# Performance work log

Measured on AMD Instinct MI355X. Metric: run time of the kernel, lower is better.

The kernel has to match this reference:

```python
import jax, jax.numpy as jnp
import numpy as np

S = 8192        # seq_length
H2 = 1024       # 2 * lstm_hidden_size
A = 2048        # attention_hidden_size
E = 768         # embedding_dim == pos_embedding_dim


def _bahdanau_weights(sentence, length, ctx, W_s, b_s, W_c, b_c, v, b_v):
    # sentence: [1, S, H2], ctx: [1, E_ctx]
    u = jnp.einsum('bsh,ha->bsa', sentence, W_s) + b_s \
        + (ctx @ W_c + b_c)[:, None, :]                    # [1, S, A]
    e = jnp.einsum('bsa,a->bs', jnp.tanh(u), v) + b_v       # [1, S]
    mask = jnp.arange(S)[None, :] >= length[:, None]        # [1, S] key mask
    e = jnp.where(mask, -jnp.inf, e)
    all_inf = jnp.all(mask, axis=1)                         # [1]
    # guard fully-masked rows so softmax stays finite, then zero them (matches torch)
    e_safe = jnp.where(all_inf[:, None], jnp.zeros_like(e), e)
    w = jax.nn.softmax(e_safe, axis=1)
    return jnp.where(all_inf[:, None], 0.0, w)              # [1, S]


def setup_inputs() -> dict:
    key = jax.random.key(0)
    ks = jax.random.split(key, 24)
    f = jax.random.normal
    sc_s = 1.0 / np.sqrt(H2)
    sc_c = 1.0 / np.sqrt(E)
    sc_v = 1.0 / np.sqrt(A)
    inp = {
        'sentence': f(ks[0], (1, S, H2), jnp.float32),
        'length': jax.random.randint(ks[1], (1,), 0, S),
        'pos_embedding': f(ks[2], (1, E), jnp.float32),
        'cardinal_phrase_embedding': f(ks[3], (1, E), jnp.float32),
        'headline_embedding': f(ks[4], (1, E), jnp.float32),
    }
    i = 5
    for tag in ('p', 'c', 'h'):
        inp[f'W_sent_{tag}'] = f(ks[i], (H2, A), jnp.float32) * sc_s; i += 1
        inp[f'b_sent_{tag}'] = f(ks[i], (A,), jnp.float32) * sc_s; i += 1
        inp[f'W_ctx_{tag}'] = f(ks[i], (E, A), jnp.float32) * sc_c; i += 1
        inp[f'b_ctx_{tag}'] = f(ks[i], (A,), jnp.float32) * sc_c; i += 1
        inp[f'v_{tag}'] = f(ks[i], (A,), jnp.float32) * sc_v; i += 1
        inp[f'bv_{tag}'] = f(ks[i], (), jnp.float32) * sc_v; i += 1
    return inp


def reference(sentence, length, pos_embedding, cardinal_phrase_embedding,
              headline_embedding,
              W_sent_p, b_sent_p, W_ctx_p, b_ctx_p, v_p, bv_p,
              W_sent_c, b_sent_c, W_ctx_c, b_ctx_c, v_c, bv_c,
              W_sent_h, b_sent_h, W_ctx_h, b_ctx_h, v_h, bv_h):
    w_pos = _bahdanau_weights(sentence, length, pos_embedding,
                              W_sent_p, b_sent_p, W_ctx_p, b_ctx_p, v_p, bv_p)
    w_card = _bahdanau_weights(sentence, length, cardinal_phrase_embedding,
                               W_sent_c, b_sent_c, W_ctx_c, b_ctx_c, v_c, bv_c)
    w_head = _bahdanau_weights(sentence, length, headline_embedding,
                               W_sent_h, b_sent_h, W_ctx_h, b_ctx_h, v_h, bv_h)
    fused = (w_pos + w_card + w_head) / 3.0                 # [1, S]
    return jnp.einsum('bs,bsh->bh', fused, sentence)        # [1, H2]
```

## Files before the change

kernel.cpp:

```cpp
#include <hip/hip_runtime.h>
#include <hip/hip_bf16.h>
#include <stdint.h>


namespace {

constexpr int S = 8192;
constexpr int H = 1024;
constexpr int A = 2048;
constexpr int E = 768;

typedef __bf16 bf16x8 __attribute__((ext_vector_type(8)));
typedef float f32x4 __attribute__((ext_vector_type(4)));

__device__ __forceinline__ void gl_lds16(const void* g, void* l) {
  __builtin_amdgcn_global_load_lds(
      (const __attribute__((address_space(1))) void*)g,
      (__attribute__((address_space(3))) void*)l, 16, 0, 0);
}

__global__ __launch_bounds__(256)
void k_prep(const float* __restrict__ sentence, __bf16* __restrict__ sentB,
            const float* __restrict__ Wp, const float* __restrict__ Wc_s,
            const float* __restrict__ Wh, __bf16* __restrict__ WtB,
            const float* __restrict__ ctx_p, const float* __restrict__ ctx_c,
            const float* __restrict__ ctx_h,
            const float* __restrict__ Wcx_p, const float* __restrict__ Wcx_c,
            const float* __restrict__ Wcx_h,
            const float* __restrict__ bs_p, const float* __restrict__ bs_c,
            const float* __restrict__ bs_h,
            const float* __restrict__ bc_p, const float* __restrict__ bc_c,
            const float* __restrict__ bc_h,
            float* __restrict__ ctxb) {
  __shared__ float tile[64][65];
  int b = blockIdx.x;
  int t = threadIdx.x;

  if (b < 4096) {
    int g = b * 256 + t;
    const float4* s4 = (const float4*)sentence + (size_t)g * 2;
    float4 a = s4[0], c = s4[1];
    bf16x8 o;
    o[0] = (__bf16)a.x; o[1] = (__bf16)a.y; o[2] = (__bf16)a.z; o[3] = (__bf16)a.w;
    o[4] = (__bf16)c.x; o[5] = (__bf16)c.y; o[6] = (__bf16)c.z; o[7] = (__bf16)c.w;
    *((bf16x8*)sentB + g) = o;
  } else if (b < 5632) {
    int r = b - 4096;
    int head = r >> 9; r &= 511;
    const float* W = head == 0 ? Wp : (head == 1 ? Wc_s : Wh);
    __bf16* dst = WtB + (size_t)head * A * H;
    int a0 = (r & 31) * 64;
    int k0 = (r >> 5) * 64;
#pragma unroll
    for (int i = 0; i < 16; ++i) {
      int idx = t + i * 256;
      int rr = idx >> 6, cc = idx & 63;
      tile[cc][rr] = W[(size_t)(k0 + rr) * A + a0 + cc];
    }
    __syncthreads();
#pragma unroll
    for (int i = 0; i < 16; ++i) {
      int idx = t + i * 256;
      int al = idx >> 6, kl = idx & 63;
      dst[(size_t)(a0 + al) * H + k0 + kl] = (__bf16)tile[al][kl];
    }
  } else {
    int r = b - 5632;
    int head = r / 192; r %= 192;
    int ablk = r & 7;
    int echk = r >> 3;
    const float* ctx = head == 0 ? ctx_p : (head == 1 ? ctx_c : ctx_h);
    const float* Wc  = head == 0 ? Wcx_p : (head == 1 ? Wcx_c : Wcx_h);
    int a = ablk * 256 + t;
    float s = 0.f;
    int e0 = echk * 32;
#pragma unroll 8
    for (int e = e0; e < e0 + 32; ++e) s = fmaf(ctx[e], Wc[(size_t)e * A + a], s);
    if (echk == 0) {
      const float* bs = head == 0 ? bs_p : (head == 1 ? bs_c : bs_h);
      const float* bc = head == 0 ? bc_p : (head == 1 ? bc_c : bc_h);
      s += bs[a] + bc[a];
    }
    atomicAdd(&ctxb[head * A + a], s);
  }
}

__global__ __launch_bounds__(256)
void k_gemm_e(const __bf16* __restrict__ sentB, const __bf16* __restrict__ WtB,
              const float* __restrict__ ctxb,
              const float* __restrict__ v_p, const float* __restrict__ v_c,
              const float* __restrict__ v_h,
              const int* __restrict__ length, float* __restrict__ e_out) {
  int m0 = blockIdx.x * 128;
  int len = length[0];
  if (m0 >= len) return;
  int n0 = blockIdx.y * 128;
  int head = blockIdx.z;
  const float* v  = head == 0 ? v_p : (head == 1 ? v_c : v_h);
  const __bf16* Wt = WtB + (size_t)head * A * H;
  const float* cb = ctxb + head * A;
  float* e_h = e_out + head * S;

  __shared__ __align__(16) __bf16 lsA[128 * 32];
  __shared__ __align__(16) __bf16 lsB[128 * 32];
  __shared__ float e_part[128];

  int tid = threadIdx.x;
  if (tid < 128) e_part[tid] = 0.f;

  int lane = tid & 63;
  int wave = tid >> 6;
  int wm = wave >> 1, wn = wave & 1;
  int quad = lane >> 4, l16 = lane & 15;

  f32x4 acc[4][4];
#pragma unroll
  for (int i = 0; i < 4; ++i)
#pragma unroll
    for (int j = 0; j < 4; ++j) acc[i][j] = (f32x4){0.f, 0.f, 0.f, 0.f};

  const __bf16* gA0 = sentB + (size_t)(m0 + (tid >> 2)) * H + ((tid & 3) * 8);
  const __bf16* gA1 = gA0 + (size_t)64 * H;
  const __bf16* gB0 = Wt + (size_t)(n0 + (tid >> 2)) * H + ((tid & 3) * 8);
  const __bf16* gB1 = gB0 + (size_t)64 * H;

  for (int k0 = 0; k0 < H; k0 += 32) {
    __syncthreads();
    gl_lds16(gA0 + k0, lsA + tid * 8);
    gl_lds16(gA1 + k0, lsA + 2048 + tid * 8);
    gl_lds16(gB0 + k0, lsB + tid * 8);
    gl_lds16(gB1 + k0, lsB + 2048 + tid * 8);
    __syncthreads();

    bf16x8 af[4], bfv[4];
#pragma unroll
    for (int i = 0; i < 4; ++i) {
      af[i]  = *(const bf16x8*)&lsA[(wm * 64 + i * 16 + l16) * 32 + quad * 8];
      bfv[i] = *(const bf16x8*)&lsB[(wn * 64 + i * 16 + l16) * 32 + quad * 8];
    }
#pragma unroll
    for (int i = 0; i < 4; ++i)
#pragma unroll
      for (int j = 0; j < 4; ++j)
        acc[i][j] = __builtin_amdgcn_mfma_f32_16x16x32_bf16(af[i], bfv[j], acc[i][j], 0, 0, 0);
  }

  float vj[4], cbj[4];
#pragma unroll
  for (int j = 0; j < 4; ++j) {
    int col = n0 + wn * 64 + j * 16 + l16;
    vj[j] = v[col];
    cbj[j] = cb[col];
  }
#pragma unroll
  for (int i = 0; i < 4; ++i) {
#pragma unroll
    for (int r = 0; r < 4; ++r) {
      float p = 0.f;
#pragma unroll
      for (int j = 0; j < 4; ++j) {
        float u = acc[i][j][r] + cbj[j];
        float ex = __expf(2.f * u);
        float th = 1.f - 2.f / (ex + 1.f);
        p = fmaf(th, vj[j], p);
      }
      p += __shfl_xor(p, 1);
      p += __shfl_xor(p, 2);
      p += __shfl_xor(p, 4);
      p += __shfl_xor(p, 8);
      if (l16 == 0) atomicAdd(&e_part[wm * 64 + i * 16 + quad * 4 + r], p);
    }
  }
  __syncthreads();
  if (tid < 128) atomicAdd(&e_h[m0 + tid], e_part[tid]);
}

__global__ void k_stats(const float* __restrict__ e_arr, const int* __restrict__ length,
                        float* __restrict__ stats) {
  int head = blockIdx.x;
  const float* e_h = e_arr + head * S;
  int len = min(max(length[0], 0), S);
  int tid = threadIdx.x;
  __shared__ float red[4];
  __shared__ float bmax;

  float m = -3.4e38f;
  for (int s = tid; s < len; s += 256) m = fmaxf(m, e_h[s]);
#pragma unroll
  for (int o = 32; o >= 1; o >>= 1) m = fmaxf(m, __shfl_xor(m, o));
  if ((tid & 63) == 0) red[tid >> 6] = m;
  __syncthreads();
  if (tid == 0) bmax = fmaxf(fmaxf(red[0], red[1]), fmaxf(red[2], red[3]));
  __syncthreads();
  float mm = bmax;

  float ss = 0.f;
  for (int s = tid; s < len; s += 256) ss += __expf(e_h[s] - mm);
#pragma unroll
  for (int o = 32; o >= 1; o >>= 1) ss += __shfl_xor(ss, o);
  __syncthreads();
  if ((tid & 63) == 0) red[tid >> 6] = ss;
  __syncthreads();
  if (tid == 0) {
    stats[head * 2 + 0] = mm;
    stats[head * 2 + 1] = red[0] + red[1] + red[2] + red[3];
  }
}

__global__ void k_out(const float* __restrict__ sent, const float* __restrict__ e_arr,
                      const float* __restrict__ stats, const int* __restrict__ length,
                      float* __restrict__ out) {
  int len = min(max(length[0], 0), S);
  int r0 = blockIdx.x * 32;
  if (r0 >= len) return;
  int col = threadIdx.x * 4;
  int rend = min(r0 + 32, len);
  float m0 = stats[0], s0 = stats[1];
  float m1 = stats[2], s1 = stats[3];
  float m2 = stats[4], s2 = stats[5];
  float4 acc = {0.f, 0.f, 0.f, 0.f};
  for (int r = r0; r < rend; ++r) {
    float w = (__expf(e_arr[r] - m0) / s0 +
               __expf(e_arr[S + r] - m1) / s1 +
               __expf(e_arr[2 * S + r] - m2) / s2) * (1.f / 3.f);
    float4 x = *(const float4*)(sent + (size_t)r * H + col);
    acc.x = fmaf(w, x.x, acc.x);
    acc.y = fmaf(w, x.y, acc.y);
    acc.z = fmaf(w, x.z, acc.z);
    acc.w = fmaf(w, x.w, acc.w);
  }
  atomicAdd(&out[col + 0], acc.x);
  atomicAdd(&out[col + 1], acc.y);
  atomicAdd(&out[col + 2], acc.z);
  atomicAdd(&out[col + 3], acc.w);
}

}

extern "C" void kernel_launch(void* const* d_in, const int* in_sizes, int n_in,
                              void* d_out, int out_size, void* d_ws, size_t ws_size,
                              hipStream_t stream) {
  const float* sentence = (const float*)d_in[0];
  const int* length     = (const int*)d_in[1];
  const float* ctx_p = (const float*)d_in[2];
  const float* ctx_c = (const float*)d_in[3];
  const float* ctx_h = (const float*)d_in[4];
  const float* W_s[3] = {(const float*)d_in[5],  (const float*)d_in[11], (const float*)d_in[17]};
  const float* b_s[3] = {(const float*)d_in[6],  (const float*)d_in[12], (const float*)d_in[18]};
  const float* W_c[3] = {(const float*)d_in[7],  (const float*)d_in[13], (const float*)d_in[19]};
  const float* b_c[3] = {(const float*)d_in[8],  (const float*)d_in[14], (const float*)d_in[20]};
  const float* v_[3]  = {(const float*)d_in[9],  (const float*)d_in[15], (const float*)d_in[21]};
  float* out = (float*)d_out;

  char* ws = (char*)d_ws;
  __bf16* sentB = (__bf16*)(ws);
  __bf16* WtB   = (__bf16*)(ws + 16777216);
  float* ctxb   = (float*)(ws + 29360128);
  float* e_arr  = (float*)(ws + 29384704);
  float* stats  = (float*)(ws + 29483008);

  hipMemsetAsync(ctxb, 0, (A * 3 + S * 3) * sizeof(float), stream);
  hipMemsetAsync(out, 0, out_size * sizeof(float), stream);

  k_prep<<<6208, 256, 0, stream>>>(sentence, sentB,
                                   W_s[0], W_s[1], W_s[2], WtB,
                                   ctx_p, ctx_c, ctx_h,
                                   W_c[0], W_c[1], W_c[2],
                                   b_s[0], b_s[1], b_s[2],
                                   b_c[0], b_c[1], b_c[2], ctxb);
  k_gemm_e<<<dim3(S / 128, A / 128, 3), 256, 0, stream>>>(sentB, WtB, ctxb,
                                                          v_[0], v_[1], v_[2], length, e_arr);
  k_stats<<<3, 256, 0, stream>>>(e_arr, length, stats);
  k_out<<<S / 32, 256, 0, stream>>>(sentence, e_arr, stats, length, out);
}
```

Before: 233.6 us.

## Triple-buffer GEMM loads, skip masked rows in prep, fold stats into output kernel

The GEMM main loop now uses a three-stage LDS ring with async global-to-LDS loads and a single waitcnt+barrier per k-step, so loads overlap MFMA work. The prep kernel skips bf16 conversion of sentence rows beyond the padded length and zeroes the output in an extra block, which replaces a memset. The separate stats kernel is removed: every output block recomputes the softmax max and sum over all three heads, and per-row weights are computed once into shared memory. This saves launches and the conversion traffic for masked rows, at the cost of redundant reduction reads in each of many output blocks.

Result: no change. 234.3 us (+0.3%).

```diff
diff --git a/kernel.cpp b/kernel.cpp
--- a/kernel.cpp
+++ b/kernel.cpp
@@ -31,12 +31,16 @@
             const float* __restrict__ bs_h,
             const float* __restrict__ bc_p, const float* __restrict__ bc_c,
             const float* __restrict__ bc_h,
-            float* __restrict__ ctxb) {
+            float* __restrict__ ctxb,
+            const int* __restrict__ length, float* __restrict__ out, int n_out) {
   __shared__ float tile[64][65];
   int b = blockIdx.x;
   int t = threadIdx.x;
 
   if (b < 4096) {
+    int len = min(max(length[0], 0), S);
+    int lenp = (len + 127) & ~127;
+    if (b * 2 >= lenp) return;
     int g = b * 256 + t;
     const float4* s4 = (const float4*)sentence + (size_t)g * 2;
     float4 a = s4[0], c = s4[1];
@@ -64,7 +68,7 @@
       int al = idx >> 6, kl = idx & 63;
       dst[(size_t)(a0 + al) * H + k0 + kl] = (__bf16)tile[al][kl];
     }
-  } else {
+  } else if (b < 6208) {
     int r = b - 5632;
     int head = r / 192; r %= 192;
     int ablk = r & 7;
@@ -82,6 +86,9 @@
       s += bs[a] + bc[a];
     }
     atomicAdd(&ctxb[head * A + a], s);
+  } else {
+    float4 z = {0.f, 0.f, 0.f, 0.f};
+    for (int i = t; i * 4 < n_out; i += 256) ((float4*)out)[i] = z;
   }
 }
 
@@ -92,7 +99,7 @@
               const float* __restrict__ v_h,
               const int* __restrict__ length, float* __restrict__ e_out) {
   int m0 = blockIdx.x * 128;
-  int len = length[0];
+  int len = min(max(length[0], 0), S);
   if (m0 >= len) return;
   int n0 = blockIdx.y * 128;
   int head = blockIdx.z;
@@ -101,8 +108,8 @@
   const float* cb = ctxb + head * A;
   float* e_h = e_out + head * S;
 
-  __shared__ __align__(16) __bf16 lsA[128 * 32];
-  __shared__ __align__(16) __bf16 lsB[128 * 32];
+  __shared__ __align__(16) __bf16 lsA[3 * 4096];
+  __shared__ __align__(16) __bf16 lsB[3 * 4096];
   __shared__ float e_part[128];
 
   int tid = threadIdx.x;
@@ -124,26 +131,45 @@
   const __bf16* gB0 = Wt + (size_t)(n0 + (tid >> 2)) * H + ((tid & 3) * 8);
   const __bf16* gB1 = gB0 + (size_t)64 * H;
 
-  for (int k0 = 0; k0 < H; k0 += 32) {
-    __syncthreads();
-    gl_lds16(gA0 + k0, lsA + tid * 8);
-    gl_lds16(gA1 + k0, lsA + 2048 + tid * 8);
-    gl_lds16(gB0 + k0, lsB + tid * 8);
-    gl_lds16(gB1 + k0, lsB + 2048 + tid * 8);
-    __syncthreads();
-
-    bf16x8 af[4], bfv[4];
-#pragma unroll
-    for (int i = 0; i < 4; ++i) {
-      af[i]  = *(const bf16x8*)&lsA[(wm * 64 + i * 16 + l16) * 32 + quad * 8];
-      bfv[i] = *(const bf16x8*)&lsB[(wn * 64 + i * 16 + l16) * 32 + quad * 8];
-    }
-#pragma unroll
-    for (int i = 0; i < 4; ++i)
-#pragma unroll
-      for (int j = 0; j < 4; ++j)
-        acc[i][j] = __builtin_amdgcn_mfma_f32_16x16x32_bf16(af[i], bfv[j], acc[i][j], 0, 0, 0);
-  }
+#define STAGE(bufi, kk)                                           \
+  do {                                                            \
+    gl_lds16(gA0 + (kk), lsA + (bufi) * 4096 + tid * 8);          \
+    gl_lds16(gA1 + (kk), lsA + (bufi) * 4096 + 2048 + tid * 8);   \
+    gl_lds16(gB0 + (kk), lsB + (bufi) * 4096 + tid * 8);          \
+    gl_lds16(gB1 + (kk), lsB + (bufi) * 4096 + 2048 + tid * 8);   \
+  } while (0)
+
+#define COMPUTE(bufi)                                                                     \
+  do {                                                                                    \
+    bf16x8 af[4], bfv[4];                                                                 \
+    _Pragma("unroll")                                                                     \
+    for (int i = 0; i < 4; ++i) {                                                         \
+      af[i]  = *(const bf16x8*)&lsA[(bufi) * 4096 + (wm * 64 + i * 16 + l16) * 32 + quad * 8]; \
+      bfv[i] = *(const bf16x8*)&lsB[(bufi) * 4096 + (wn * 64 + i * 16 + l16) * 32 + quad * 8]; \
+    }                                                                                     \
+    _Pragma("unroll")                                                                     \
+    for (int i = 0; i < 4; ++i)                                                           \
+      _Pragma("unroll")                                                                   \
+      for (int j = 0; j < 4; ++j)                                                         \
+        acc[i][j] = __builtin_amdgcn_mfma_f32_16x16x32_bf16(af[i], bfv[j], acc[i][j], 0, 0, 0); \
+  } while (0)
+
+  STAGE(0, 0);
+  STAGE(1, 32);
+  int cur = 0, nxt = 2;
+#pragma unroll 1
+  for (int t = 0; t < 31; ++t) {
+    asm volatile("s_waitcnt vmcnt(4)\n\ts_barrier" ::: "memory");
+    if (t < 30) STAGE(nxt, (t + 2) * 32);
+    COMPUTE(cur);
+    cur = cur == 2 ? 0 : cur + 1;
+    nxt = nxt == 2 ? 0 : nxt + 1;
+  }
+  asm volatile("s_waitcnt vmcnt(0)\n\ts_barrier" ::: "memory");
+  COMPUTE(cur);
+
+#undef STAGE
+#undef COMPUTE
 
   float vj[4], cbj[4];
 #pragma unroll
@@ -175,54 +201,57 @@
   if (tid < 128) atomicAdd(&e_h[m0 + tid], e_part[tid]);
 }
 
-__global__ void k_stats(const float* __restrict__ e_arr, const int* __restrict__ length,
-                        float* __restrict__ stats) {
-  int head = blockIdx.x;
-  const float* e_h = e_arr + head * S;
+__global__ void k_out(const float* __restrict__ sent, const float* __restrict__ e_arr,
+                      const int* __restrict__ length, float* __restrict__ out) {
   int len = min(max(length[0], 0), S);
+  int r0 = blockIdx.x * 16;
+  if (r0 >= len) return;
   int tid = threadIdx.x;
-  __shared__ float red[4];
-  __shared__ float bmax;
-
-  float m = -3.4e38f;
-  for (int s = tid; s < len; s += 256) m = fmaxf(m, e_h[s]);
-#pragma unroll
-  for (int o = 32; o >= 1; o >>= 1) m = fmaxf(m, __shfl_xor(m, o));
-  if ((tid & 63) == 0) red[tid >> 6] = m;
-  __syncthreads();
-  if (tid == 0) bmax = fmaxf(fmaxf(red[0], red[1]), fmaxf(red[2], red[3]));
-  __syncthreads();
-  float mm = bmax;
-
-  float ss = 0.f;
-  for (int s = tid; s < len; s += 256) ss += __expf(e_h[s] - mm);
-#pragma unroll
-  for (int o = 32; o >= 1; o >>= 1) ss += __shfl_xor(ss, o);
-  __syncthreads();
-  if ((tid & 63) == 0) red[tid >> 6] = ss;
-  __syncthreads();
-  if (tid == 0) {
-    stats[head * 2 + 0] = mm;
-    stats[head * 2 + 1] = red[0] + red[1] + red[2] + red[3];
-  }
-}
-
-__global__ void k_out(const float* __restrict__ sent, const float* __restrict__ e_arr,
-                      const float* __restrict__ stats, const int* __restrict__ length,
-                      float* __restrict__ out) {
-  int len = min(max(length[0], 0), S);
-  int r0 = blockIdx.x * 32;
-  if (r0 >= len) return;
-  int col = threadIdx.x * 4;
-  int rend = min(r0 + 32, len);
-  float m0 = stats[0], s0 = stats[1];
-  float m1 = stats[2], s1 = stats[3];
-  float m2 = stats[4], s2 = stats[5];
+
+  __shared__ float red[3][4];
+  __shared__ float sstat[6];
+  __shared__ float wrow[16];
+
+#pragma unroll
+  for (int h = 0; h < 3; ++h) {
+    const float* e_h = e_arr + h * S;
+    float m = -3.4e38f;
+    for (int s = tid; s < len; s += 256) m = fmaxf(m, e_h[s]);
+#pragma unroll
+    for (int o = 32; o >= 1; o >>= 1) m = fmaxf(m, __shfl_xor(m, o));
+    if ((tid & 63) == 0) red[h][tid >> 6] = m;
+  }
+  __syncthreads();
+  if (tid < 3) sstat[tid * 2] = fmaxf(fmaxf(red[tid][0], red[tid][1]),
+                                      fmaxf(red[tid][2], red[tid][3]));
+  __syncthreads();
+#pragma unroll
+  for (int h = 0; h < 3; ++h) {
+    const float* e_h = e_arr + h * S;
+    float mm = sstat[h * 2];
+    float ss = 0.f;
+    for (int s = tid; s < len; s += 256) ss += __expf(e_h[s] - mm);
+#pragma unroll
+    for (int o = 32; o >= 1; o >>= 1) ss += __shfl_xor(ss, o);
+    if ((tid & 63) == 0) red[h][tid >> 6] = ss;
+  }
+  __syncthreads();
+  if (tid < 3) sstat[tid * 2 + 1] = red[tid][0] + red[tid][1] + red[tid][2] + red[tid][3];
+  __syncthreads();
+
+  if (tid < 16 && r0 + tid < len) {
+    int r = r0 + tid;
+    wrow[tid] = (__expf(e_arr[r] - sstat[0]) / sstat[1] +
+                 __expf(e_arr[S + r] - sstat[2]) / sstat[3] +
+                 __expf(e_arr[2 * S + r] - sstat[4]) / sstat[5]) * (1.f / 3.f);
+  }
+  __syncthreads();
+
+  int col = tid * 4;
+  int rend = min(r0 + 16, len);
   float4 acc = {0.f, 0.f, 0.f, 0.f};
   for (int r = r0; r < rend; ++r) {
-    float w = (__expf(e_arr[r] - m0) / s0 +
-               __expf(e_arr[S + r] - m1) / s1 +
-               __expf(e_arr[2 * S + r] - m2) / s2) * (1.f / 3.f);
+    float w = wrow[r - r0];
     float4 x = *(const float4*)(sent + (size_t)r * H + col);
     acc.x = fmaf(w, x.x, acc.x);
     acc.y = fmaf(w, x.y, acc.y);
@@ -257,19 +286,17 @@
   __bf16* WtB   = (__bf16*)(ws + 16777216);
   float* ctxb   = (float*)(ws + 29360128);
   float* e_arr  = (float*)(ws + 29384704);
-  float* stats  = (float*)(ws + 29483008);
 
   hipMemsetAsync(ctxb, 0, (A * 3 + S * 3) * sizeof(float), stream);
-  hipMemsetAsync(out, 0, out_size * sizeof(float), stream);
-
-  k_prep<<<6208, 256, 0, stream>>>(sentence, sentB,
+
+  k_prep<<<6209, 256, 0, stream>>>(sentence, sentB,
                                    W_s[0], W_s[1], W_s[2], WtB,
                                    ctx_p, ctx_c, ctx_h,
                                    W_c[0], W_c[1], W_c[2],
                                    b_s[0], b_s[1], b_s[2],
-                                   b_c[0], b_c[1], b_c[2], ctxb);
+                                   b_c[0], b_c[1], b_c[2], ctxb,
+                                   length, out, out_size);
   k_gemm_e<<<dim3(S / 128, A / 128, 3), 256, 0, stream>>>(sentB, WtB, ctxb,
                                                           v_[0], v_[1], v_[2], length, e_arr);
-  k_stats<<<3, 256, 0, stream>>>(e_arr, length, stats);
-  k_out<<<S / 32, 256, 0, stream>>>(sentence, e_arr, stats, length, out);
-}
+  k_out<<<S / 16, 256, 0, stream>>>(sentence, e_arr, length, out);
+}
```
